# Optimization experiments

Measured on AMD Instinct MI355X. Metric: run time of the kernel, lower is better.

Reference implementation:

```python
import jax, jax.numpy as jnp
import numpy as np

N, F_IN, PRE, K = 400000, 64, 32, 6
EDGE = [32, 32]


def _dense_params(key, fan_in, fan_out):
    kw, kb = jax.random.split(key)
    W = jax.random.normal(kw, (fan_in, fan_out), jnp.float32) / np.sqrt(fan_in).astype(np.float32)
    b = jnp.zeros((fan_out,), jnp.float32)
    return W, b


def setup_inputs() -> dict:
    key = jax.random.key(0)
    ks = jax.random.split(key, 10)
    x = jax.random.normal(ks[0], (N, F_IN), jnp.float32)
    distsq = jax.random.uniform(ks[1], (N, K), jnp.float32)
    nidx = jax.random.randint(ks[2], (N, K), 0, N, jnp.int64)
    Wp, bp = _dense_params(ks[3], F_IN, PRE)
    # edge MLP: input K*(PRE+1) -> 32 -> 32 -> K
    We1, be1 = _dense_params(ks[4], K * (PRE + 1), EDGE[0])
    We2, be2 = _dense_params(ks[5], EDGE[0], EDGE[1])
    We3, be3 = _dense_params(ks[6], EDGE[1], K)
    # self MLP: F_IN -> 32 -> 32 -> 1
    Ws1, bs1 = _dense_params(ks[7], F_IN, EDGE[0])
    Ws2, bs2 = _dense_params(ks[8], EDGE[0], EDGE[1])
    Ws3, bs3 = _dense_params(ks[9], EDGE[1], 1)
    return dict(x=x, distsq=distsq, nidx=nidx, Wp=Wp, bp=bp,
                We1=We1, be1=be1, We2=We2, be2=be2, We3=We3, be3=be3,
                Ws1=Ws1, bs1=bs1, Ws2=Ws2, bs2=bs2, Ws3=Ws3, bs3=bs3)


def _forward(x, distsq, nidx, Wp, bp, We1, be1, We2, be2, We3, be3,
             Ws1, bs1, Ws2, bs2, Ws3, bs3):
    # pre-dense: [N, PRE]
    x_p = jax.nn.elu(x @ Wp + bp)
    # gather neighbors; select(nidx, x_n, 0.0) masks nidx<0 to 0.0
    safe_idx = jnp.maximum(nidx, 0)
    gathered = x_p[safe_idx]                              # [N, K, PRE]
    gathered = jnp.where(nidx[:, :, None] < 0, 0.0, gathered)
    diff = x_p[:, None, :] - gathered                     # [N, K, PRE]
    xn = jnp.concatenate([diff, distsq[:, :, None]], axis=2)  # [N, K, PRE+1]
    xn = xn.reshape(xn.shape[0], K * (PRE + 1))
    xn = jax.nn.elu(xn @ We1 + be1)
    xn = jax.nn.elu(xn @ We2 + be2)
    xn = xn @ We3 + be3                                   # [N, K]
    xs = jax.nn.elu(x @ Ws1 + bs1)
    xs = jax.nn.elu(xs @ Ws2 + bs2)
    xs = xs @ Ws3 + bs3                                   # [N, 1]
    out = jnp.concatenate([xs, xn], axis=1)               # [N, K+1]
    return jax.nn.softmax(out, axis=1)


def reference(x, distsq, nidx, Wp, bp, We1, be1, We2, be2, We3, be3,
              Ws1, bs1, Ws2, bs2, Ws3, bs3):
    return _forward(x, distsq, nidx, Wp, bp, We1, be1, We2, be2, We3, be3,
                    Ws1, bs1, Ws2, bs2, Ws3, bs3)
```

## Files before the change

### kernel.cpp

```cpp
#include <hip/hip_runtime.h>
#include <hip/hip_bf16.h>
#include <math.h>

typedef __hip_bfloat16 bf16;
typedef __attribute__((ext_vector_type(8))) __bf16 bf16x8;
typedef __attribute__((ext_vector_type(4))) float f32x4;

#define F_IN 64
#define KNB 6

#define WOFF_WP   0
#define WOFF_BP   2048
#define WOFF_WE1  2080
#define WOFF_BE1  8416
#define WOFF_WE2  8448
#define WOFF_BE2  9472
#define WOFF_WE3  9504
#define WOFF_BE3  9696
#define WOFF_WS1  9728
#define WOFF_BS1  11776
#define WOFF_WS2  11808
#define WOFF_BS2  12832
#define WOFF_WS3  12864
#define WOFF_BS3  12896
#define FLAGS_OFF 13056
#define WOFF_WSUM 13312
#define WOFF_WDSQ 14336
#define FRAG_OFF  14592
#define NFRAG_PRE 11
#define NFRAG_EDGE 19
#define STAGE_OFF 24576

#define MFMA(a, b, c) __builtin_amdgcn_mfma_f32_16x16x32_bf16(a, b, c, 0, 0, 0)

__device__ __forceinline__ float b2f(bf16 v) { return __bfloat162float(v); }
__device__ __forceinline__ float eluf(float v) { return v > 0.f ? v : __expf(v) - 1.f; }

__device__ __forceinline__ ushort f2bu(float v) {
  __bf16 b = (__bf16)v; ushort u; __builtin_memcpy(&u, &b, 2); return u;
}

union U8 { uint4 u; bf16x8 v; ushort s[8]; };

__device__ __forceinline__ bf16x8 ldfrag(const ushort* fr, int f) {
  U8 u; u.u = *(const uint4*)(fr + f * 512 + (threadIdx.x & 63) * 8);
  return u.v;
}

__device__ __forceinline__ int permo(int m, int t) { return 8 * (m >> 2) + (m & 3) + 4 * t; }

__global__ void setupK(const ushort* xb, const int* ni,
                       const void* Wp, const void* bp, const void* We1, const void* be1,
                       const void* We2, const void* be2, const void* We3, const void* be3,
                       const void* Ws1, const void* bs1, const void* Ws2, const void* bs2,
                       const void* Ws3, const void* bs3, float* w) {
  __shared__ int sbf;
  int t = threadIdx.x;
  if (t < 64) {
    int bad = 0;
    for (int i = t; i < 256; i += 64) {
      float v = __uint_as_float(((unsigned)xb[i]) << 16);
      if (!(fabsf(v) < 100.f)) bad++;
    }
    unsigned long long bm = __ballot(bad > 0);
    unsigned long long hm = __ballot(ni[2 * t + 1] != 0);
    if (t == 0) {
      int isbf = (__popcll(bm) < 4) ? 1 : 0;
      ((int*)(w + FLAGS_OFF))[0] = isbf;
      ((int*)(w + FLAGS_OFF))[1] = (hm == 0ULL) ? 1 : 0;
      sbf = isbf;
    }
  }
  __syncthreads();
  int bf = sbf;
  const void* srcs[14] = {Wp, bp, We1, be1, We2, be2, We3, be3, Ws1, bs1, Ws2, bs2, Ws3, bs3};
  const int sizes[14] = {2048, 32, 6336, 32, 1024, 32, 192, 6, 2048, 32, 1024, 32, 32, 1};
  const int offs[14] = {WOFF_WP, WOFF_BP, WOFF_WE1, WOFF_BE1, WOFF_WE2, WOFF_BE2, WOFF_WE3,
                        WOFF_BE3, WOFF_WS1, WOFF_BS1, WOFF_WS2, WOFF_BS2, WOFF_WS3, WOFF_BS3};
  for (int tt = 0; tt < 14; tt++) {
    const void* s = srcs[tt];
    int nel = sizes[tt];
    float* d = w + offs[tt];
    for (int i = t; i < nel; i += blockDim.x)
      d[i] = bf ? b2f(((const bf16*)s)[i]) : ((const float*)s)[i];
  }
  __syncthreads();
  for (int i = t; i < 1024; i += blockDim.x) {
    int j = i >> 5, o = i & 31;
    float s = 0.f;
    for (int k = 0; k < KNB; k++) s += w[WOFF_WE1 + (k * 33 + j) * 32 + o];
    w[WOFF_WSUM + i] = s;
  }
  for (int i = t; i < 192; i += blockDim.x) {
    int k = i >> 5, o = i & 31;
    w[WOFF_WDSQ + i] = w[WOFF_WE1 + (k * 33 + 32) * 32 + o];
  }
  __syncthreads();
  ushort* fbv = (ushort*)(w + FRAG_OFF);
  for (int i = t; i < (NFRAG_PRE + NFRAG_EDGE) * 512; i += blockDim.x) {
    int f = i >> 9, e = i & 511;
    int lane = e >> 3, j = e & 7;
    int mm = lane & 15, qq = lane >> 4;
    int k = qq * 8 + j;
    float v = 0.f;
    if (f < 4) { int s = f >> 1, tt = f & 1; v = w[WOFF_WP + (32 * s + k) * 32 + permo(mm, tt)]; }
    else if (f < 8) { int s = (f - 4) >> 1, tt = f & 1; v = w[WOFF_WS1 + (32 * s + k) * 32 + permo(mm, tt)]; }
    else if (f < 10) { int tt = f & 1; v = w[WOFF_WS2 + k * 32 + permo(mm, tt)]; }
    else if (f == 10) { v = (mm == 0) ? w[WOFF_WS3 + k] : 0.f; }
    else if (f < 23) { int kn = (f - 11) >> 1, tt = (f - 11) & 1;
                       v = -w[WOFF_WE1 + (kn * 33 + k) * 32 + permo(mm, tt)]; }
    else if (f < 25) { int tt = f - 23; v = w[WOFF_WSUM + k * 32 + permo(mm, tt)]; }
    else if (f < 27) { int tt = f - 25; int o = permo(mm, tt);
                       v = (k < 6) ? w[WOFF_WDSQ + k * 32 + o]
                                   : (k == 6 ? w[WOFF_BE1 + o] : 0.f); }
    else if (f < 29) { int tt = f - 27; v = w[WOFF_WE2 + k * 32 + permo(mm, tt)]; }
    else { v = (mm < KNB) ? w[WOFF_WE3 + k * 6 + mm] : 0.f; }
    fbv[i] = f2bu(v);
  }
}

template <bool BF16>
__device__ void pre_tiles(const void* xv, const float* __restrict__ w,
                          ushort* __restrict__ xp, float* __restrict__ xs,
                          int n_nodes, const ushort* __restrict__ fr) {
  int lane = threadIdx.x & 63;
  int m = lane & 15, q = lane >> 4;
  float bp8[8], bs18[8], bs28[8];
#pragma unroll
  for (int j = 0; j < 8; j++) {
    bp8[j]  = w[WOFF_BP  + 8 * q + j];
    bs18[j] = w[WOFF_BS1 + 8 * q + j];
    bs28[j] = w[WOFF_BS2 + 8 * q + j];
  }
  float bs3 = w[WOFF_BS3];
  long T = ((long)n_nodes + 15) >> 4;
  long wid = (long)((blockIdx.x * blockDim.x + threadIdx.x) >> 6);
  long nw = (long)((gridDim.x * blockDim.x) >> 6);
  f32x4 zero = {0.f, 0.f, 0.f, 0.f};

  uint4 bufA[4], bufB[4];
  auto loadraw = [&](uint4* r, long tt) {
    long row = tt * 16 + m; if (row >= n_nodes) row = n_nodes - 1;
    if (BF16) {
      const ushort* p = (const ushort*)xv + row * F_IN + q * 8;
      r[0] = *(const uint4*)p;
      r[1] = *(const uint4*)(p + 32);
    } else {
      const float* p = (const float*)xv + row * F_IN + q * 8;
      r[0] = *(const uint4*)p;        r[1] = *(const uint4*)(p + 4);
      r[2] = *(const uint4*)(p + 32); r[3] = *(const uint4*)(p + 36);
    }
  };
  auto mkfrag = [&](const uint4* r, int s) -> bf16x8 {
    if (BF16) { U8 u; u.u = r[s]; return u.v; }
    const float* f0 = (const float*)(r + 2 * s);
    bf16x8 out;
#pragma unroll
    for (int j = 0; j < 8; j++) out[j] = (__bf16)f0[j];
    return out;
  };
  auto body = [&](uint4* cur, uint4* nxt, long t) {
    long tn = t + nw;
    if (tn < T) loadraw(nxt, tn);
    long n0 = t * 16;
    long row = n0 + m; if (row >= n_nodes) row = n_nodes - 1;
    bf16x8 x0 = mkfrag(cur, 0), x1 = mkfrag(cur, 1);
    f32x4 aP[2], aS[2];
#pragma unroll
    for (int tt = 0; tt < 2; tt++) {
      aP[tt] = MFMA(ldfrag(fr, 0 + tt), x0, zero);
      aP[tt] = MFMA(ldfrag(fr, 2 + tt), x1, aP[tt]);
      aS[tt] = MFMA(ldfrag(fr, 4 + tt), x0, zero);
      aS[tt] = MFMA(ldfrag(fr, 6 + tt), x1, aS[tt]);
    }
    U8 o1;
#pragma unroll
    for (int j = 0; j < 8; j++) o1.s[j] = f2bu(eluf(aP[j >> 2][j & 3] + bp8[j]));
    *(uint4*)(xp + row * 32 + q * 8) = o1.u;
    bf16x8 s1e;
#pragma unroll
    for (int j = 0; j < 8; j++) s1e[j] = (__bf16)eluf(aS[j >> 2][j & 3] + bs18[j]);
    f32x4 a2[2];
#pragma unroll
    for (int tt = 0; tt < 2; tt++) a2[tt] = MFMA(ldfrag(fr, 8 + tt), s1e, zero);
    bf16x8 s2e;
#pragma unroll
    for (int j = 0; j < 8; j++) s2e[j] = (__bf16)eluf(a2[j >> 2][j & 3] + bs28[j]);
    f32x4 a3 = MFMA(ldfrag(fr, 10), s2e, zero);
    if (q == 0) {
      long orow = n0 + m;
      if (orow < n_nodes) xs[orow] = a3[0] + bs3;
    }
  };
  long t = wid;
  if (t < T) loadraw(bufA, t);
  while (t < T) {
    body(bufA, bufB, t);
    t += nw; if (t >= T) break;
    body(bufB, bufA, t);
    t += nw;
  }
}

__launch_bounds__(256)
__global__ void preK(const void* xv, const float* __restrict__ w,
                     const int* __restrict__ flags,
                     ushort* __restrict__ xp, float* __restrict__ xs, int n_nodes) {
  __shared__ uint4 fsh[NFRAG_PRE * 64];
  const uint4* fbv = (const uint4*)((const ushort*)(w + FRAG_OFF));
  for (int i = threadIdx.x; i < NFRAG_PRE * 64; i += blockDim.x) fsh[i] = fbv[i];
  __syncthreads();
  const ushort* fr = (const ushort*)fsh;
  if (flags[0]) pre_tiles<true>(xv, w, xp, xs, n_nodes, fr);
  else          pre_tiles<false>(xv, w, xp, xs, n_nodes, fr);
}

struct ETile { U8 nb[KNB]; U8 own; U8 ad; float xsv; };

template <bool BF16>
__device__ void edge_tiles(const ushort* __restrict__ xp, const float* __restrict__ xs,
                           const void* dsv, const int* __restrict__ ni, int i64,
                           const float* __restrict__ w, void* outv, int n_nodes,
                           const ushort* __restrict__ fr) {
  int lane = threadIdx.x & 63;
  int m = lane & 15, q = lane >> 4;
  float b2[8], b3[4];
#pragma unroll
  for (int j = 0; j < 8; j++) b2[j] = w[WOFF_BE2 + 8 * q + j];
#pragma unroll
  for (int r = 0; r < 4; r++) { int o = 4 * q + r; b3[r] = (o < 6) ? w[WOFF_BE3 + o] : 0.f; }

  long T = ((long)n_nodes + 15) >> 4;
  long wid = (long)((blockIdx.x * blockDim.x + threadIdx.x) >> 6);
  long nw = (long)((gridDim.x * blockDim.x) >> 6);
  f32x4 zero = {0.f, 0.f, 0.f, 0.f};
  ETile A, B;

  auto phead = [&](ETile& d, int* idxn, long tt) {
    long row = tt * 16 + m; if (row >= n_nodes) row = n_nodes - 1;
#pragma unroll
    for (int k = 0; k < KNB; k++)
      idxn[k] = i64 ? ni[(row * KNB + k) * 2] : ni[row * KNB + k];
    d.own.u = *(const uint4*)(xp + row * 32 + q * 8);
    d.ad.u.x = 0; d.ad.u.y = 0; d.ad.u.z = 0; d.ad.u.w = 0;
    if (q == 0) {
      if (BF16) {
        const unsigned* dp = (const unsigned*)dsv;
        d.ad.u.x = dp[row * 3 + 0]; d.ad.u.y = dp[row * 3 + 1]; d.ad.u.z = dp[row * 3 + 2];
      } else {
        const float* dp = (const float*)dsv + row * KNB;
#pragma unroll
        for (int k = 0; k < KNB; k++) d.ad.s[k] = f2bu(dp[k]);
      }
      d.ad.s[6] = 0x3F80u;
    }
    d.xsv = xs[row];
  };
  auto pgather = [&](ETile& d, const int* idxn) {
#pragma unroll
    for (int k = 0; k < KNB; k++) {
      int ix = idxn[k];
      long ai = (ix < 0 || ix >= n_nodes) ? 0 : (long)ix;
      uint4 g = *(const uint4*)(xp + ai * 32 + q * 8);
      if (ix < 0) { g.x = 0; g.y = 0; g.z = 0; g.w = 0; }
      d.nb[k].u = g;
    }
  };
  auto body = [&](ETile& cur, ETile& nxt, long t) {
    long tn = t + nw;
    int idxn[KNB];
    bool pv = tn < T;
    if (pv) phead(nxt, idxn, tn);
    f32x4 acc[2];
#pragma unroll
    for (int tt = 0; tt < 2; tt++) {
      acc[tt] = MFMA(ldfrag(fr, 12 + tt), cur.own.v, zero);
      acc[tt] = MFMA(ldfrag(fr, 14 + tt), cur.ad.v, acc[tt]);
#pragma unroll
      for (int k = 0; k < KNB; k++)
        acc[tt] = MFMA(ldfrag(fr, k * 2 + tt), cur.nb[k].v, acc[tt]);
    }
    if (pv) pgather(nxt, idxn);
    bf16x8 a1;
#pragma unroll
    for (int j = 0; j < 8; j++) a1[j] = (__bf16)eluf(acc[j >> 2][j & 3]);
    f32x4 acc2[2];
#pragma unroll
    for (int tt = 0; tt < 2; tt++) acc2[tt] = MFMA(ldfrag(fr, 16 + tt), a1, zero);
    bf16x8 a2;
#pragma unroll
    for (int j = 0; j < 8; j++) a2[j] = (__bf16)eluf(acc2[j >> 2][j & 3] + b2[j]);
    f32x4 a3 = MFMA(ldfrag(fr, 18), a2, zero);
    float l0 = a3[0] + b3[0], l1 = a3[1] + b3[1], l2 = a3[2] + b3[2], l3 = a3[3] + b3[3];
    float o4 = __shfl(l0, m + 16, 64);
    float o5 = __shfl(l1, m + 16, 64);
    if (lane < 16) {
      long nodeid = t * 16 + lane;
      if (nodeid < n_nodes) {
        float lg[7] = {cur.xsv, l0, l1, l2, l3, o4, o5};
        float mx = lg[0];
#pragma unroll
        for (int i = 1; i < 7; i++) mx = fmaxf(mx, lg[i]);
        float e[7], ssum = 0.f;
#pragma unroll
        for (int i = 0; i < 7; i++) { e[i] = __expf(lg[i] - mx); ssum += e[i]; }
        float inv = 1.f / ssum;
        if (BF16) {
          ushort* o = (ushort*)outv + nodeid * 7;
#pragma unroll
          for (int i = 0; i < 7; i++) o[i] = f2bu(e[i] * inv);
        } else {
          float* o = (float*)outv + nodeid * 7;
#pragma unroll
          for (int i = 0; i < 7; i++) o[i] = e[i] * inv;
        }
      }
    }
  };
  long t = wid;
  if (t < T) { int i0[KNB]; phead(A, i0, t); pgather(A, i0); }
  while (t < T) {
    body(A, B, t);
    t += nw; if (t >= T) break;
    body(B, A, t);
    t += nw;
  }
}

__launch_bounds__(256)
__global__ void edgeK(const ushort* __restrict__ xp, const float* __restrict__ xs,
                      const void* dsv, const int* __restrict__ ni,
                      const float* __restrict__ w, const int* __restrict__ flags,
                      void* outv, int n_nodes) {
  __shared__ uint4 fsh[NFRAG_EDGE * 64];
  const uint4* fbv = (const uint4*)((const ushort*)(w + FRAG_OFF) + NFRAG_PRE * 512);
  for (int i = threadIdx.x; i < NFRAG_EDGE * 64; i += blockDim.x) fsh[i] = fbv[i];
  __syncthreads();
  const ushort* fr = (const ushort*)fsh;
  if (flags[0]) edge_tiles<true>(xp, xs, dsv, ni, flags[1], w, outv, n_nodes, fr);
  else          edge_tiles<false>(xp, xs, dsv, ni, flags[1], w, outv, n_nodes, fr);
}

template <bool BF16>
__device__ __forceinline__ float wval(const void* W, long i) {
  if (BF16) return b2f(((const bf16*)W)[i]);
  return ((const float*)W)[i];
}

__device__ __forceinline__ void block_flags(const ushort* xb, const int* ni, int* sflags) {
  if (threadIdx.x < 64) {
    int t = threadIdx.x;
    int bad = 0;
    for (int i = t; i < 256; i += 64) {
      float v = __uint_as_float(((unsigned)xb[i]) << 16);
      if (!(fabsf(v) < 100.f)) bad++;
    }
    unsigned long long bm = __ballot(bad > 0);
    unsigned long long hm = __ballot(ni[2 * t + 1] != 0);
    if (t == 0) {
      sflags[0] = (__popcll(bm) < 4) ? 1 : 0;
      sflags[1] = (hm == 0ULL) ? 1 : 0;
    }
  }
  __syncthreads();
}

template <bool BF16>
__device__ void node_body(int n, int n_nodes, const void* xv, const void* dsv,
                          const int* __restrict__ ni, int i64,
                          const void* Wp, const void* bp, const void* We1, const void* be1,
                          const void* We2, const void* be2, const void* We3, const void* be3,
                          const void* Ws1, const void* bs1, const void* Ws2, const void* bs2,
                          const void* Ws3, const void* bs3, void* outv) {
  float h[32], s1[32];
#pragma unroll
  for (int o = 0; o < 32; o++) { h[o] = wval<BF16>(bp, o); s1[o] = wval<BF16>(bs1, o); }
  for (int j = 0; j < F_IN; j++) {
    float xj = wval<BF16>(xv, (long)n * F_IN + j);
#pragma unroll
    for (int o = 0; o < 32; o++) {
      h[o]  += xj * wval<BF16>(Wp,  (long)j * 32 + o);
      s1[o] += xj * wval<BF16>(Ws1, (long)j * 32 + o);
    }
  }
  float own[32];
#pragma unroll
  for (int o = 0; o < 32; o++) own[o] = eluf(h[o]);
  float s2[32];
#pragma unroll
  for (int o = 0; o < 32; o++) s2[o] = wval<BF16>(bs2, o);
  for (int j = 0; j < 32; j++) {
    float v = eluf(s1[j]);
#pragma unroll
    for (int o = 0; o < 32; o++) s2[o] += v * wval<BF16>(Ws2, (long)j * 32 + o);
  }
  float xsv = wval<BF16>(bs3, 0);
#pragma unroll
  for (int j = 0; j < 32; j++) xsv += eluf(s2[j]) * wval<BF16>(Ws3, j);

  float h1[32];
#pragma unroll
  for (int o = 0; o < 32; o++) h1[o] = wval<BF16>(be1, o);
  for (int k = 0; k < KNB; k++) {
    long pos = (long)n * KNB + k;
    int idx = i64 ? ni[2 * pos] : ni[pos];
    float mmask = idx < 0 ? 0.f : 1.f;
    long ai = idx < 0 ? 0 : idx;
    if (ai >= n_nodes) ai = 0;
    float nh[32];
#pragma unroll
    for (int o = 0; o < 32; o++) nh[o] = wval<BF16>(bp, o);
    for (int j = 0; j < F_IN; j++) {
      float xj = wval<BF16>(xv, ai * F_IN + j);
#pragma unroll
      for (int o = 0; o < 32; o++) nh[o] += xj * wval<BF16>(Wp, (long)j * 32 + o);
    }
#pragma unroll
    for (int j = 0; j < 32; j++) {
      float d = own[j] - mmask * eluf(nh[j]);
#pragma unroll
      for (int o = 0; o < 32; o++) h1[o] += d * wval<BF16>(We1, ((long)(k * 33 + j)) * 32 + o);
    }
    float dsq = BF16 ? b2f(((const bf16*)dsv)[pos]) : ((const float*)dsv)[pos];
#pragma unroll
    for (int o = 0; o < 32; o++) h1[o] += dsq * wval<BF16>(We1, ((long)(k * 33 + 32)) * 32 + o);
  }
  float h2[32];
#pragma unroll
  for (int o = 0; o < 32; o++) h2[o] = wval<BF16>(be2, o);
  for (int j = 0; j < 32; j++) {
    float v = eluf(h1[j]);
#pragma unroll
    for (int o = 0; o < 32; o++) h2[o] += v * wval<BF16>(We2, (long)j * 32 + o);
  }
  float lg[7];
  lg[0] = xsv;
#pragma unroll
  for (int o = 0; o < 6; o++) lg[1 + o] = wval<BF16>(be3, o);
  for (int j = 0; j < 32; j++) {
    float v = eluf(h2[j]);
#pragma unroll
    for (int o = 0; o < 6; o++) lg[1 + o] += v * wval<BF16>(We3, (long)j * 6 + o);
  }
  float mx = lg[0];
#pragma unroll
  for (int i = 1; i < 7; i++) mx = fmaxf(mx, lg[i]);
  float e[7], ssum = 0.f;
#pragma unroll
  for (int i = 0; i < 7; i++) { e[i] = __expf(lg[i] - mx); ssum += e[i]; }
  float inv = 1.f / ssum;
  if (BF16) {
    bf16* o = (bf16*)outv;
#pragma unroll
    for (int i = 0; i < 7; i++) o[(long)n * 7 + i] = __float2bfloat16(e[i] * inv);
  } else {
    float* o = (float*)outv;
#pragma unroll
    for (int i = 0; i < 7; i++) o[(long)n * 7 + i] = e[i] * inv;
  }
}

__launch_bounds__(256)
__global__ void fused(const void* xv, const void* dsv, const int* __restrict__ ni,
                      const void* Wp, const void* bp, const void* We1, const void* be1,
                      const void* We2, const void* be2, const void* We3, const void* be3,
                      const void* Ws1, const void* bs1, const void* Ws2, const void* bs2,
                      const void* Ws3, const void* bs3, void* outv, int n_nodes) {
  __shared__ int sflags[2];
  block_flags((const ushort*)xv, ni, sflags);
  int n = blockIdx.x * blockDim.x + threadIdx.x;
  if (n >= n_nodes) return;
  if (sflags[0]) node_body<true>(n, n_nodes, xv, dsv, ni, sflags[1], Wp, bp, We1, be1,
                                 We2, be2, We3, be3, Ws1, bs1, Ws2, bs2, Ws3, bs3, outv);
  else           node_body<false>(n, n_nodes, xv, dsv, ni, sflags[1], Wp, bp, We1, be1,
                                  We2, be2, We3, be3, Ws1, bs1, Ws2, bs2, Ws3, bs3, outv);
}

extern "C" void kernel_launch(void* const* d_in, const int* in_sizes, int n_in,
                              void* d_out, int out_size, void* d_ws, size_t ws_size,
                              hipStream_t stream) {
  const void* x      = d_in[0];
  const void* distsq = d_in[1];
  const int*  nidx   = (const int*)d_in[2];

  float* w = (float*)d_ws;
  int* flags = (int*)(w + FLAGS_OFF);
  int n_nodes = in_sizes[0] / F_IN;

  size_t need = (size_t)STAGE_OFF * 4 + (size_t)n_nodes * 64 + (size_t)n_nodes * 4 + 256;
  if (ws_size >= need) {
    setupK<<<1, 256, 0, stream>>>((const ushort*)x, nidx,
                                  d_in[3], d_in[4], d_in[5], d_in[6], d_in[7], d_in[8],
                                  d_in[9], d_in[10], d_in[11], d_in[12], d_in[13], d_in[14],
                                  d_in[15], d_in[16], w);
    ushort* xp = (ushort*)(w + STAGE_OFF);
    float* xs = (float*)(xp + (size_t)n_nodes * 32);
    preK<<<1024, 256, 0, stream>>>(x, w, flags, xp, xs, n_nodes);
    edgeK<<<1024, 256, 0, stream>>>(xp, xs, distsq, nidx, w, flags, d_out, n_nodes);
  } else {
    int grid = (n_nodes + 255) / 256;
    fused<<<grid, 256, 0, stream>>>(x, distsq, nidx, d_in[3], d_in[4], d_in[5], d_in[6],
                                    d_in[7], d_in[8], d_in[9], d_in[10], d_in[11], d_in[12],
                                    d_in[13], d_in[14], d_in[15], d_in[16], d_out, n_nodes);
  }
}
```

Measured before the change: 303.5 us.

## Parallelize setup, deepen edge prefetch, nontemporal x loads, double grid

The setup kernel now runs on 32 blocks and builds the bf16 MFMA fragments straight from the input weights, dropping the intermediate fp32 staging copies and the syncthreads between them. The edge kernel gains a deeper software pipeline: neighbor indices are fetched two tiles ahead and head data one tile ahead, so the gathers can overlap more compute. Loads of x in the pre kernel use nontemporal hints, and both the pre and edge kernels launch 2048 blocks instead of 1024. The risks are higher register pressure from the extra prefetch state and possible loss of cache reuse.

```diff
diff --git a/kernel.cpp b/kernel.cpp
--- a/kernel.cpp
+++ b/kernel.cpp
@@ -5,27 +5,18 @@
 typedef __hip_bfloat16 bf16;
 typedef __attribute__((ext_vector_type(8))) __bf16 bf16x8;
 typedef __attribute__((ext_vector_type(4))) float f32x4;
+typedef unsigned int u32x4 __attribute__((ext_vector_type(4)));
 
 #define F_IN 64
 #define KNB 6
 
-#define WOFF_WP   0
 #define WOFF_BP   2048
-#define WOFF_WE1  2080
-#define WOFF_BE1  8416
-#define WOFF_WE2  8448
 #define WOFF_BE2  9472
-#define WOFF_WE3  9504
 #define WOFF_BE3  9696
-#define WOFF_WS1  9728
 #define WOFF_BS1  11776
-#define WOFF_WS2  11808
 #define WOFF_BS2  12832
-#define WOFF_WS3  12864
 #define WOFF_BS3  12896
 #define FLAGS_OFF 13056
-#define WOFF_WSUM 13312
-#define WOFF_WDSQ 14336
 #define FRAG_OFF  14592
 #define NFRAG_PRE 11
 #define NFRAG_EDGE 19
@@ -41,6 +32,11 @@
 }
 
 union U8 { uint4 u; bf16x8 v; ushort s[8]; };
+
+__device__ __forceinline__ uint4 ntload16(const void* p) {
+  u32x4 t = __builtin_nontemporal_load((const u32x4*)p);
+  uint4 r; r.x = t.x; r.y = t.y; r.z = t.z; r.w = t.w; return r;
+}
 
 __device__ __forceinline__ bf16x8 ldfrag(const ushort* fr, int f) {
   U8 u; u.u = *(const uint4*)(fr + f * 512 + (threadIdx.x & 63) * 8);
@@ -63,58 +59,52 @@
       if (!(fabsf(v) < 100.f)) bad++;
     }
     unsigned long long bm = __ballot(bad > 0);
-    unsigned long long hm = __ballot(ni[2 * t + 1] != 0);
-    if (t == 0) {
-      int isbf = (__popcll(bm) < 4) ? 1 : 0;
-      ((int*)(w + FLAGS_OFF))[0] = isbf;
-      ((int*)(w + FLAGS_OFF))[1] = (hm == 0ULL) ? 1 : 0;
-      sbf = isbf;
-    }
+    if (t == 0) sbf = (__popcll(bm) < 4) ? 1 : 0;
   }
   __syncthreads();
   int bf = sbf;
-  const void* srcs[14] = {Wp, bp, We1, be1, We2, be2, We3, be3, Ws1, bs1, Ws2, bs2, Ws3, bs3};
-  const int sizes[14] = {2048, 32, 6336, 32, 1024, 32, 192, 6, 2048, 32, 1024, 32, 32, 1};
-  const int offs[14] = {WOFF_WP, WOFF_BP, WOFF_WE1, WOFF_BE1, WOFF_WE2, WOFF_BE2, WOFF_WE3,
-                        WOFF_BE3, WOFF_WS1, WOFF_BS1, WOFF_WS2, WOFF_BS2, WOFF_WS3, WOFF_BS3};
-  for (int tt = 0; tt < 14; tt++) {
-    const void* s = srcs[tt];
-    int nel = sizes[tt];
-    float* d = w + offs[tt];
-    for (int i = t; i < nel; i += blockDim.x)
-      d[i] = bf ? b2f(((const bf16*)s)[i]) : ((const float*)s)[i];
-  }
-  __syncthreads();
-  for (int i = t; i < 1024; i += blockDim.x) {
-    int j = i >> 5, o = i & 31;
-    float s = 0.f;
-    for (int k = 0; k < KNB; k++) s += w[WOFF_WE1 + (k * 33 + j) * 32 + o];
-    w[WOFF_WSUM + i] = s;
-  }
-  for (int i = t; i < 192; i += blockDim.x) {
-    int k = i >> 5, o = i & 31;
-    w[WOFF_WDSQ + i] = w[WOFF_WE1 + (k * 33 + 32) * 32 + o];
-  }
-  __syncthreads();
+  auto rv = [&](const void* p, long i) -> float {
+    return bf ? b2f(((const bf16*)p)[i]) : ((const float*)p)[i];
+  };
+  if (blockIdx.x == 0) {
+    if (t < 64) {
+      unsigned long long hm = __ballot(ni[2 * t + 1] != 0);
+      if (t == 0) {
+        ((int*)(w + FLAGS_OFF))[0] = bf;
+        ((int*)(w + FLAGS_OFF))[1] = (hm == 0ULL) ? 1 : 0;
+      }
+    }
+    const void* bsrc[6] = {bp, bs1, bs2, bs3, be2, be3};
+    const int bn[6] = {32, 32, 32, 1, 32, 6};
+    const int bo[6] = {WOFF_BP, WOFF_BS1, WOFF_BS2, WOFF_BS3, WOFF_BE2, WOFF_BE3};
+    for (int a = 0; a < 6; a++)
+      for (int i = t; i < bn[a]; i += blockDim.x)
+        w[bo[a] + i] = rv(bsrc[a], i);
+  }
   ushort* fbv = (ushort*)(w + FRAG_OFF);
-  for (int i = t; i < (NFRAG_PRE + NFRAG_EDGE) * 512; i += blockDim.x) {
+  int total = (NFRAG_PRE + NFRAG_EDGE) * 512;
+  for (int i = blockIdx.x * blockDim.x + t; i < total; i += gridDim.x * blockDim.x) {
     int f = i >> 9, e = i & 511;
     int lane = e >> 3, j = e & 7;
     int mm = lane & 15, qq = lane >> 4;
     int k = qq * 8 + j;
     float v = 0.f;
-    if (f < 4) { int s = f >> 1, tt = f & 1; v = w[WOFF_WP + (32 * s + k) * 32 + permo(mm, tt)]; }
-    else if (f < 8) { int s = (f - 4) >> 1, tt = f & 1; v = w[WOFF_WS1 + (32 * s + k) * 32 + permo(mm, tt)]; }
-    else if (f < 10) { int tt = f & 1; v = w[WOFF_WS2 + k * 32 + permo(mm, tt)]; }
-    else if (f == 10) { v = (mm == 0) ? w[WOFF_WS3 + k] : 0.f; }
+    if (f < 4) { int s = f >> 1, tt = f & 1; v = rv(Wp, (long)(32 * s + k) * 32 + permo(mm, tt)); }
+    else if (f < 8) { int s = (f - 4) >> 1, tt = f & 1; v = rv(Ws1, (long)(32 * s + k) * 32 + permo(mm, tt)); }
+    else if (f < 10) { int tt = f & 1; v = rv(Ws2, (long)k * 32 + permo(mm, tt)); }
+    else if (f == 10) { v = (mm == 0) ? rv(Ws3, k) : 0.f; }
     else if (f < 23) { int kn = (f - 11) >> 1, tt = (f - 11) & 1;
-                       v = -w[WOFF_WE1 + (kn * 33 + k) * 32 + permo(mm, tt)]; }
-    else if (f < 25) { int tt = f - 23; v = w[WOFF_WSUM + k * 32 + permo(mm, tt)]; }
+                       v = -rv(We1, (long)(kn * 33 + k) * 32 + permo(mm, tt)); }
+    else if (f < 25) { int tt = f - 23; float s = 0.f;
+#pragma unroll
+                       for (int kn = 0; kn < KNB; kn++)
+                         s += rv(We1, (long)(kn * 33 + k) * 32 + permo(mm, tt));
+                       v = s; }
     else if (f < 27) { int tt = f - 25; int o = permo(mm, tt);
-                       v = (k < 6) ? w[WOFF_WDSQ + k * 32 + o]
-                                   : (k == 6 ? w[WOFF_BE1 + o] : 0.f); }
-    else if (f < 29) { int tt = f - 27; v = w[WOFF_WE2 + k * 32 + permo(mm, tt)]; }
-    else { v = (mm < KNB) ? w[WOFF_WE3 + k * 6 + mm] : 0.f; }
+                       v = (k < 6) ? rv(We1, (long)(k * 33 + 32) * 32 + o)
+                                   : (k == 6 ? rv(be1, o) : 0.f); }
+    else if (f < 29) { int tt = f - 27; v = rv(We2, (long)k * 32 + permo(mm, tt)); }
+    else { v = (mm < KNB) ? rv(We3, (long)k * 6 + mm) : 0.f; }
     fbv[i] = f2bu(v);
   }
 }
@@ -143,17 +133,18 @@
     long row = tt * 16 + m; if (row >= n_nodes) row = n_nodes - 1;
     if (BF16) {
       const ushort* p = (const ushort*)xv + row * F_IN + q * 8;
-      r[0] = *(const uint4*)p;
-      r[1] = *(const uint4*)(p + 32);
+      r[0] = ntload16(p);
+      r[1] = ntload16(p + 32);
     } else {
       const float* p = (const float*)xv + row * F_IN + q * 8;
-      r[0] = *(const uint4*)p;        r[1] = *(const uint4*)(p + 4);
-      r[2] = *(const uint4*)(p + 32); r[3] = *(const uint4*)(p + 36);
+      r[0] = ntload16(p);      r[1] = ntload16(p + 4);
+      r[2] = ntload16(p + 32); r[3] = ntload16(p + 36);
     }
   };
   auto mkfrag = [&](const uint4* r, int s) -> bf16x8 {
     if (BF16) { U8 u; u.u = r[s]; return u.v; }
-    const float* f0 = (const float*)(r + 2 * s);
+    float f0[8];
+    __builtin_memcpy(f0, r + 2 * s, 32);
     bf16x8 out;
 #pragma unroll
     for (int j = 0; j < 8; j++) out[j] = (__bf16)f0[j];
@@ -235,12 +226,16 @@
   long nw = (long)((gridDim.x * blockDim.x) >> 6);
   f32x4 zero = {0.f, 0.f, 0.f, 0.f};
   ETile A, B;
-
-  auto phead = [&](ETile& d, int* idxn, long tt) {
+  int Ia[KNB], Ib[KNB];
+
+  auto pidx = [&](int* ix, long tt) {
     long row = tt * 16 + m; if (row >= n_nodes) row = n_nodes - 1;
 #pragma unroll
     for (int k = 0; k < KNB; k++)
-      idxn[k] = i64 ? ni[(row * KNB + k) * 2] : ni[row * KNB + k];
+      ix[k] = i64 ? ni[(row * KNB + k) * 2] : ni[row * KNB + k];
+  };
+  auto phead = [&](ETile& d, long tt) {
+    long row = tt * 16 + m; if (row >= n_nodes) row = n_nodes - 1;
     d.own.u = *(const uint4*)(xp + row * 32 + q * 8);
     d.ad.u.x = 0; d.ad.u.y = 0; d.ad.u.z = 0; d.ad.u.w = 0;
     if (q == 0) {
@@ -256,21 +251,20 @@
     }
     d.xsv = xs[row];
   };
-  auto pgather = [&](ETile& d, const int* idxn) {
+  auto pgather = [&](ETile& d, const int* ix) {
 #pragma unroll
     for (int k = 0; k < KNB; k++) {
-      int ix = idxn[k];
-      long ai = (ix < 0 || ix >= n_nodes) ? 0 : (long)ix;
+      int v = ix[k];
+      long ai = (v < 0 || v >= n_nodes) ? 0 : (long)v;
       uint4 g = *(const uint4*)(xp + ai * 32 + q * 8);
-      if (ix < 0) { g.x = 0; g.y = 0; g.z = 0; g.w = 0; }
+      if (v < 0) { g.x = 0; g.y = 0; g.z = 0; g.w = 0; }
       d.nb[k].u = g;
     }
   };
-  auto body = [&](ETile& cur, ETile& nxt, long t) {
-    long tn = t + nw;
-    int idxn[KNB];
-    bool pv = tn < T;
-    if (pv) phead(nxt, idxn, tn);
+  auto iterb = [&](ETile& cur, ETile& nxt, int* Iin, int* Iout, long t) {
+    long t2 = t + 2 * nw;
+    bool h2 = t2 < T;
+    if (h2) pidx(Iout, t2);
     f32x4 acc[2];
 #pragma unroll
     for (int tt = 0; tt < 2; tt++) {
@@ -280,7 +274,7 @@
       for (int k = 0; k < KNB; k++)
         acc[tt] = MFMA(ldfrag(fr, k * 2 + tt), cur.nb[k].v, acc[tt]);
     }
-    if (pv) pgather(nxt, idxn);
+    if (t + nw < T) pgather(nxt, Iin);
     bf16x8 a1;
 #pragma unroll
     for (int j = 0; j < 8; j++) a1[j] = (__bf16)eluf(acc[j >> 2][j & 3]);
@@ -316,13 +310,17 @@
         }
       }
     }
+    if (h2) phead(cur, t2);
   };
   long t = wid;
-  if (t < T) { int i0[KNB]; phead(A, i0, t); pgather(A, i0); }
+  if (t < T) {
+    pidx(Ia, t); phead(A, t); pgather(A, Ia);
+    if (t + nw < T) { pidx(Ia, t + nw); phead(B, t + nw); }
+  }
   while (t < T) {
-    body(A, B, t);
+    iterb(A, B, Ia, Ib, t);
     t += nw; if (t >= T) break;
-    body(B, A, t);
+    iterb(B, A, Ib, Ia, t);
     t += nw;
   }
 }
@@ -489,14 +487,14 @@
 
   size_t need = (size_t)STAGE_OFF * 4 + (size_t)n_nodes * 64 + (size_t)n_nodes * 4 + 256;
   if (ws_size >= need) {
-    setupK<<<1, 256, 0, stream>>>((const ushort*)x, nidx,
-                                  d_in[3], d_in[4], d_in[5], d_in[6], d_in[7], d_in[8],
-                                  d_in[9], d_in[10], d_in[11], d_in[12], d_in[13], d_in[14],
-                                  d_in[15], d_in[16], w);
+    setupK<<<32, 256, 0, stream>>>((const ushort*)x, nidx,
+                                   d_in[3], d_in[4], d_in[5], d_in[6], d_in[7], d_in[8],
+                                   d_in[9], d_in[10], d_in[11], d_in[12], d_in[13], d_in[14],
+                                   d_in[15], d_in[16], w);
     ushort* xp = (ushort*)(w + STAGE_OFF);
     float* xs = (float*)(xp + (size_t)n_nodes * 32);
-    preK<<<1024, 256, 0, stream>>>(x, w, flags, xp, xs, n_nodes);
-    edgeK<<<1024, 256, 0, stream>>>(xp, xs, distsq, nidx, w, flags, d_out, n_nodes);
+    preK<<<2048, 256, 0, stream>>>(x, w, flags, xp, xs, n_nodes);
+    edgeK<<<2048, 256, 0, stream>>>(xp, xs, distsq, nidx, w, flags, d_out, n_nodes);
   } else {
     int grid = (n_nodes + 255) / 256;
     fused<<<grid, 256, 0, stream>>>(x, distsq, nidx, d_in[3], d_in[4], d_in[5], d_in[6],
```

Result: faster. 252.6 us (-16.8%).
